# Optimization experiments

Measured on AMD Instinct MI355X. Metric: run time of the kernel, lower is better.

## Reference

```python
import jax, jax.numpy as jnp
import numpy as np
import math

B, C, H, L, E = 4, 4, 8, 512, 128  # L == win_size + 1


def setup_inputs() -> dict:
    key = jax.random.key(0)
    kq, kk, kv, ks = jax.random.split(key, 4)
    queries = jax.random.normal(kq, (B, C, H, L, E), jnp.float32)
    keys = jax.random.normal(kk, (B, C, H, L, E), jnp.float32)
    values = jax.random.normal(kv, (B, C, H, L, E), jnp.float32)
    sigma = jax.random.normal(ks, (B, C, H, L), jnp.float32)
    # triangular causal mask: True above the diagonal (masked out)
    tri = jnp.triu(jnp.ones((L, L), dtype=bool), k=1)
    attn_mask = jnp.broadcast_to(tri[None, None, None], (B, 1, 1, L, L))
    return {"queries": queries, "keys": keys, "values": values,
            "sigma": sigma, "attn_mask": attn_mask}


def reference(queries, keys, values, sigma, attn_mask):
    Bq, Cq, Hq, Lq, Eq = queries.shape
    scale = 1.0 / math.sqrt(Eq)
    # scores: [B,C,H,L,L]
    scores = jnp.einsum("bchle,bchme->bchlm", queries, keys)
    scores = jnp.where(attn_mask, -jnp.inf, scores)
    attn = scale * scores

    # Gaussian prior from learned sigma
    sig = jax.nn.sigmoid(sigma * 5.0) + 1e-5
    sig = jnp.power(3.0, sig) - 1.0            # [B,C,H,L]
    sig = sig[..., None]                        # [B,C,H,L,1]
    idx = jnp.arange(Lq, dtype=queries.dtype)
    dist = jnp.abs(idx[:, None] - idx[None, :])  # [L,L]
    inv_norm = 1.0 / (math.sqrt(2.0 * math.pi) * sig)
    prior = inv_norm * jnp.exp(-(dist ** 2) / (2.0 * sig ** 2))  # [B,C,H,L,L]

    series = jax.nn.softmax(attn, axis=-1)      # dropout p=0.0 -> identity
    V = jnp.einsum("bchlm,bchme->bchle", series, values)
    sigma_out = jnp.broadcast_to(sig, prior.shape)
    return V, series, prior, sigma_out
```

## Files before the change

### kernel.cpp

```cpp
#include <hip/hip_runtime.h>
#include <math.h>

#define L 512
#define E 128
#define NT 8

typedef __attribute__((ext_vector_type(8))) short bf16x8;
typedef __attribute__((ext_vector_type(4))) float f32x4;
typedef __attribute__((ext_vector_type(4))) unsigned short u16x4;

__device__ __forceinline__ unsigned short bf16_rne(float x) {
  unsigned u = __builtin_bit_cast(unsigned, x);
  unsigned r = u + 0x7FFFu + ((u >> 16) & 1u);
  return (unsigned short)(r >> 16);
}
__device__ __forceinline__ float bf16_to_f(unsigned short h) {
  unsigned u = ((unsigned)h) << 16;
  return __builtin_bit_cast(float, u);
}

__global__ __launch_bounds__(256) void prior_kernel(
    const float* __restrict__ sigma,
    float* __restrict__ prior,
    float* __restrict__ sigma_out) {
  const int half = threadIdx.x >> 7;
  const int t128 = threadIdx.x & 127;
  const int m0 = t128 * 4;
#pragma unroll 4
  for (int i = 0; i < 16; ++i) {
    const int row = blockIdx.x * 32 + i * 2 + half;
    const int l = row & (L - 1);
    const float x = sigma[row];
    const float sg = 1.0f / (1.0f + __expf(-5.0f * x)) + 1e-5f;
    const float sigp = expm1f(sg * 1.0986122886681098f);
    const float inv_norm = 0.3989422804014327f / sigp;
    const float c = -1.0f / (2.0f * sigp * sigp);

    f32x4 pr, so;
    so[0] = so[1] = so[2] = so[3] = sigp;
#pragma unroll
    for (int j = 0; j < 4; ++j) {
      float d = (float)(l - (m0 + j));
      pr[j] = inv_norm * __expf(c * d * d);
    }
    const size_t off = (size_t)row * L + m0;
    __builtin_nontemporal_store(pr, (f32x4*)(prior + off));
    __builtin_nontemporal_store(so, (f32x4*)(sigma_out + off));
  }
}

__global__ __launch_bounds__(256, 2) void attn_kernel(
    const float* __restrict__ Q,
    const float* __restrict__ K,
    const float* __restrict__ V,
    float* __restrict__ outV,
    float* __restrict__ series) {
  const int bch = blockIdx.x;
  const int qt = 7 - blockIdx.y;
  const int tid = threadIdx.x;
  const int w = tid >> 6, lane = tid & 63, r = lane & 15, g = lane >> 4;

  __shared__ char smem[47104];
  char* sK = smem;
  char* sVt = smem + 17408;
  char* sP = smem + 37888;

  const size_t base = (size_t)bch * (L * E);
  const int qbase = qt * 64;
  const float scale = 0.08838834764831845f;

  bf16x8 qh[4], ql[4];
  {
    const float* qrow = Q + base + (size_t)(qbase + 16 * w + r) * E;
#pragma unroll
    for (int ks = 0; ks < 4; ++ks) {
      const int e0 = 32 * ks + 8 * g;
      f32x4 a = *(const f32x4*)(qrow + e0);
      f32x4 b = *(const f32x4*)(qrow + e0 + 4);
#pragma unroll
      for (int j = 0; j < 4; ++j) {
        float xa = a[j] * scale;
        unsigned short ha = bf16_rne(xa);
        qh[ks][j] = (short)ha;
        ql[ks][j] = (short)bf16_rne(xa - bf16_to_f(ha));
        float xb = b[j] * scale;
        unsigned short hb = bf16_rne(xb);
        qh[ks][4 + j] = (short)hb;
        ql[ks][4 + j] = (short)bf16_rne(xb - bf16_to_f(hb));
      }
    }
  }

  f32x4 Sacc[NT][4];
  float srow[4] = {0.f, 0.f, 0.f, 0.f};
  f32x4 Oacc[8];
#pragma unroll
  for (int cb = 0; cb < 8; ++cb) Oacc[cb] = (f32x4){0.f, 0.f, 0.f, 0.f};

#pragma unroll
  for (int t = 0; t < NT; ++t) {
    if (t <= qt) {
      __syncthreads();
#pragma unroll
      for (int i = 0; i < 8; ++i) {
        int f = i * 256 + tid;
        int row = f >> 5;
        int e0 = (f & 31) * 4;
        f32x4 kv = *(const f32x4*)(K + base + (size_t)(t * 64 + row) * E + e0);
        u16x4 h4;
#pragma unroll
        for (int j = 0; j < 4; ++j) h4[j] = bf16_rne(kv[j]);
        *(u16x4*)(sK + row * 272 + e0 * 2) = h4;
      }
#pragma unroll
      for (int bb = 0; bb < 2; ++bb) {
        int bidx = tid + 256 * bb;
        int m0 = (bidx >> 5) * 4;
        int e0 = (bidx & 31) * 4;
        const float* vrow = V + base + (size_t)(t * 64 + m0) * E + e0;
        f32x4 R0 = *(const f32x4*)(vrow);
        f32x4 R1 = *(const f32x4*)(vrow + E);
        f32x4 R2 = *(const f32x4*)(vrow + 2 * E);
        f32x4 R3 = *(const f32x4*)(vrow + 3 * E);
#pragma unroll
        for (int i = 0; i < 4; ++i) {
          u16x4 wv;
          wv[0] = bf16_rne(R0[i]);
          wv[1] = bf16_rne(R1[i]);
          wv[2] = bf16_rne(R2[i]);
          wv[3] = bf16_rne(R3[i]);
          int e = e0 + i;
          int byte = e * 160 + m0 * 2;
          byte ^= ((e >> 2) & 7) << 4;
          *(u16x4*)(sVt + byte) = wv;
        }
      }
      __syncthreads();

#pragma unroll
      for (int cb = 0; cb < 4; ++cb) Sacc[t][cb] = (f32x4){0.f, 0.f, 0.f, 0.f};
#pragma unroll
      for (int ks = 0; ks < 4; ++ks) {
#pragma unroll
        for (int cb = 0; cb < 4; ++cb) {
          const int kb = (16 * cb + r) * 272 + (32 * ks + 8 * g) * 2;
          bf16x8 bh = *(const bf16x8*)(sK + kb);
          f32x4 acc = Sacc[t][cb];
          acc = __builtin_amdgcn_mfma_f32_16x16x32_bf16(qh[ks], bh, acc, 0, 0, 0);
          acc = __builtin_amdgcn_mfma_f32_16x16x32_bf16(ql[ks], bh, acc, 0, 0, 0);
          Sacc[t][cb] = acc;
        }
      }

#pragma unroll
      for (int cb = 0; cb < 4; ++cb)
#pragma unroll
        for (int reg = 0; reg < 4; ++reg) {
          float p = __expf(Sacc[t][cb][reg]);
          if (t == qt && (16 * cb + r) > (16 * w + 4 * g + reg)) p = 0.f;
          Sacc[t][cb][reg] = p;
          srow[reg] += p;
          *(unsigned short*)(sP + (16 * w + 4 * g + reg) * 144 +
                             (16 * cb + r) * 2) = bf16_rne(p);
        }
      asm volatile("s_waitcnt lgkmcnt(0)" ::: "memory");
      __builtin_amdgcn_sched_barrier(0);

#pragma unroll
      for (int ks = 0; ks < 2; ++ks) {
        bf16x8 ap =
            *(const bf16x8*)(sP + (16 * w + r) * 144 + (32 * ks + 8 * g) * 2);
#pragma unroll
        for (int cb = 0; cb < 8; ++cb) {
          int e = 16 * cb + r;
          int byte = e * 160 + (32 * ks + 8 * g) * 2;
          byte ^= ((e >> 2) & 7) << 4;
          bf16x8 bv = *(const bf16x8*)(sVt + byte);
          Oacc[cb] = __builtin_amdgcn_mfma_f32_16x16x32_bf16(ap, bv, Oacc[cb],
                                                             0, 0, 0);
        }
      }
    }
  }

  float inv[4];
#pragma unroll
  for (int off = 1; off <= 8; off <<= 1)
#pragma unroll
    for (int reg = 0; reg < 4; ++reg)
      srow[reg] += __shfl_xor(srow[reg], off, 64);
#pragma unroll
  for (int reg = 0; reg < 4; ++reg) inv[reg] = 1.0f / srow[reg];

#pragma unroll
  for (int t = 0; t < NT; ++t) {
#pragma unroll
    for (int cb = 0; cb < 4; ++cb)
#pragma unroll
      for (int reg = 0; reg < 4; ++reg) {
        size_t off = ((size_t)bch * L + qbase + 16 * w + 4 * g + reg) * L +
                     t * 64 + 16 * cb + r;
        float val = (t <= qt) ? Sacc[t][cb][reg] * inv[reg] : 0.f;
        __builtin_nontemporal_store(val, series + off);
      }
  }

#pragma unroll
  for (int cb = 0; cb < 8; ++cb)
#pragma unroll
    for (int reg = 0; reg < 4; ++reg)
      outV[base + (size_t)(qbase + 16 * w + 4 * g + reg) * E + 16 * cb + r] =
          Oacc[cb][reg] * inv[reg];
}

extern "C" void kernel_launch(void* const* d_in, const int* in_sizes, int n_in,
                              void* d_out, int out_size, void* d_ws,
                              size_t ws_size, hipStream_t stream) {
  const float* Q = (const float*)d_in[0];
  const float* K = (const float*)d_in[1];
  const float* V = (const float*)d_in[2];
  const float* sigma = (const float*)d_in[3];

  float* out = (float*)d_out;
  float* outV = out;
  float* series = out + 8388608;
  float* prior = out + 41943040;
  float* sigma_out = out + 75497472;

  attn_kernel<<<dim3(128, 8), 256, 0, stream>>>(Q, K, V, outV, series);
  prior_kernel<<<dim3(2048), 256, 0, stream>>>(sigma, prior, sigma_out);
}
```

Measured before the change: 526.6 us.

## Fuse prior computation into attention kernel and stage outputs through LDS

```diff
diff --git a/kernel.cpp b/kernel.cpp
--- a/kernel.cpp
+++ b/kernel.cpp
@@ -19,51 +19,24 @@
   return __builtin_bit_cast(float, u);
 }
 
-__global__ __launch_bounds__(256) void prior_kernel(
-    const float* __restrict__ sigma,
-    float* __restrict__ prior,
-    float* __restrict__ sigma_out) {
-  const int half = threadIdx.x >> 7;
-  const int t128 = threadIdx.x & 127;
-  const int m0 = t128 * 4;
-#pragma unroll 4
-  for (int i = 0; i < 16; ++i) {
-    const int row = blockIdx.x * 32 + i * 2 + half;
-    const int l = row & (L - 1);
-    const float x = sigma[row];
-    const float sg = 1.0f / (1.0f + __expf(-5.0f * x)) + 1e-5f;
-    const float sigp = expm1f(sg * 1.0986122886681098f);
-    const float inv_norm = 0.3989422804014327f / sigp;
-    const float c = -1.0f / (2.0f * sigp * sigp);
-
-    f32x4 pr, so;
-    so[0] = so[1] = so[2] = so[3] = sigp;
-#pragma unroll
-    for (int j = 0; j < 4; ++j) {
-      float d = (float)(l - (m0 + j));
-      pr[j] = inv_norm * __expf(c * d * d);
-    }
-    const size_t off = (size_t)row * L + m0;
-    __builtin_nontemporal_store(pr, (f32x4*)(prior + off));
-    __builtin_nontemporal_store(so, (f32x4*)(sigma_out + off));
-  }
-}
-
-__global__ __launch_bounds__(256, 2) void attn_kernel(
+__global__ __launch_bounds__(256, 3) void fused_kernel(
     const float* __restrict__ Q,
     const float* __restrict__ K,
     const float* __restrict__ V,
+    const float* __restrict__ sigma,
     float* __restrict__ outV,
-    float* __restrict__ series) {
+    float* __restrict__ series,
+    float* __restrict__ prior,
+    float* __restrict__ sigma_out) {
   const int bch = blockIdx.x;
   const int qt = 7 - blockIdx.y;
   const int tid = threadIdx.x;
   const int w = tid >> 6, lane = tid & 63, r = lane & 15, g = lane >> 4;
 
-  __shared__ char smem[47104];
+  __shared__ char smem[37888];
   char* sK = smem;
   char* sVt = smem + 17408;
-  char* sP = smem + 37888;
+  char* sP = smem;
 
   const size_t base = (size_t)bch * (L * E);
   const int qbase = qt * 64;
@@ -91,7 +64,7 @@
     }
   }
 
-  f32x4 Sacc[NT][4];
+  unsigned Sp[NT][8];
   float srow[4] = {0.f, 0.f, 0.f, 0.f};
   f32x4 Oacc[8];
 #pragma unroll
@@ -137,32 +110,46 @@
       }
       __syncthreads();
 
-#pragma unroll
-      for (int cb = 0; cb < 4; ++cb) Sacc[t][cb] = (f32x4){0.f, 0.f, 0.f, 0.f};
+      f32x4 Sacc[4];
+#pragma unroll
+      for (int cb = 0; cb < 4; ++cb) Sacc[cb] = (f32x4){0.f, 0.f, 0.f, 0.f};
 #pragma unroll
       for (int ks = 0; ks < 4; ++ks) {
 #pragma unroll
         for (int cb = 0; cb < 4; ++cb) {
           const int kb = (16 * cb + r) * 272 + (32 * ks + 8 * g) * 2;
           bf16x8 bh = *(const bf16x8*)(sK + kb);
-          f32x4 acc = Sacc[t][cb];
+          f32x4 acc = Sacc[cb];
           acc = __builtin_amdgcn_mfma_f32_16x16x32_bf16(qh[ks], bh, acc, 0, 0, 0);
           acc = __builtin_amdgcn_mfma_f32_16x16x32_bf16(ql[ks], bh, acc, 0, 0, 0);
-          Sacc[t][cb] = acc;
-        }
-      }
-
+          Sacc[cb] = acc;
+        }
+      }
+
+      unsigned short h[4][4];
 #pragma unroll
       for (int cb = 0; cb < 4; ++cb)
 #pragma unroll
         for (int reg = 0; reg < 4; ++reg) {
-          float p = __expf(Sacc[t][cb][reg]);
+          float p = __expf(Sacc[cb][reg]);
           if (t == qt && (16 * cb + r) > (16 * w + 4 * g + reg)) p = 0.f;
-          Sacc[t][cb][reg] = p;
           srow[reg] += p;
+          h[cb][reg] = bf16_rne(p);
+        }
+#pragma unroll
+      for (int cb = 0; cb < 4; ++cb) {
+        Sp[t][2 * cb + 0] = (unsigned)h[cb][0] | ((unsigned)h[cb][1] << 16);
+        Sp[t][2 * cb + 1] = (unsigned)h[cb][2] | ((unsigned)h[cb][3] << 16);
+      }
+
+      __syncthreads();
+
+#pragma unroll
+      for (int cb = 0; cb < 4; ++cb)
+#pragma unroll
+        for (int reg = 0; reg < 4; ++reg)
           *(unsigned short*)(sP + (16 * w + 4 * g + reg) * 144 +
-                             (16 * cb + r) * 2) = bf16_rne(p);
-        }
+                             (16 * cb + r) * 2) = h[cb][reg];
       asm volatile("s_waitcnt lgkmcnt(0)" ::: "memory");
       __builtin_amdgcn_sched_barrier(0);
 
@@ -192,25 +179,107 @@
 #pragma unroll
   for (int reg = 0; reg < 4; ++reg) inv[reg] = 1.0f / srow[reg];
 
+  __syncthreads();
+
+  float* sInvW = (float*)(smem + 36864) + 16 * w;
+  if (r == 0) {
+#pragma unroll
+    for (int reg = 0; reg < 4; ++reg) sInvW[4 * g + reg] = inv[reg];
+  }
+
 #pragma unroll
   for (int t = 0; t < NT; ++t) {
-#pragma unroll
-    for (int cb = 0; cb < 4; ++cb)
-#pragma unroll
-      for (int reg = 0; reg < 4; ++reg) {
-        size_t off = ((size_t)bch * L + qbase + 16 * w + 4 * g + reg) * L +
-                     t * 64 + 16 * cb + r;
-        float val = (t <= qt) ? Sacc[t][cb][reg] * inv[reg] : 0.f;
-        __builtin_nontemporal_store(val, series + off);
-      }
-  }
-
+    if (t <= qt) {
+#pragma unroll
+      for (int cb = 0; cb < 4; ++cb)
+#pragma unroll
+        for (int j = 0; j < 2; ++j) {
+          unsigned pk = Sp[t][2 * cb + j];
+          *(unsigned short*)(sP + (16 * w + 4 * g + 2 * j) * 144 +
+                             (16 * cb + r) * 2) = (unsigned short)(pk & 0xFFFF);
+          *(unsigned short*)(sP + (16 * w + 4 * g + 2 * j + 1) * 144 +
+                             (16 * cb + r) * 2) = (unsigned short)(pk >> 16);
+        }
+      asm volatile("s_waitcnt lgkmcnt(0)" ::: "memory");
+      __builtin_amdgcn_sched_barrier(0);
+#pragma unroll
+      for (int a = 0; a < 2; ++a) {
+        int rw = 8 * a + (lane >> 3);
+        float iv = sInvW[rw];
+#pragma unroll
+        for (int b = 0; b < 2; ++b) {
+          int m0 = 32 * b + (lane & 7) * 4;
+          u16x4 pv = *(const u16x4*)(sP + (16 * w + rw) * 144 + m0 * 2);
+          f32x4 o;
+          o[0] = bf16_to_f(pv[0]) * iv;
+          o[1] = bf16_to_f(pv[1]) * iv;
+          o[2] = bf16_to_f(pv[2]) * iv;
+          o[3] = bf16_to_f(pv[3]) * iv;
+          __builtin_nontemporal_store(
+              o, (f32x4*)(series + ((size_t)bch * L + qbase + 16 * w + rw) * L +
+                          t * 64 + m0));
+        }
+      }
+    } else {
+      f32x4 z = (f32x4){0.f, 0.f, 0.f, 0.f};
+#pragma unroll
+      for (int a = 0; a < 2; ++a) {
+        int rw = 8 * a + (lane >> 3);
+#pragma unroll
+        for (int b = 0; b < 2; ++b) {
+          int m0 = 32 * b + (lane & 7) * 4;
+          __builtin_nontemporal_store(
+              z, (f32x4*)(series + ((size_t)bch * L + qbase + 16 * w + rw) * L +
+                          t * 64 + m0));
+        }
+      }
+    }
+  }
+
+  __syncthreads();
+
+  float* sOw = (float*)(smem + w * 9472);
 #pragma unroll
   for (int cb = 0; cb < 8; ++cb)
 #pragma unroll
     for (int reg = 0; reg < 4; ++reg)
-      outV[base + (size_t)(qbase + 16 * w + 4 * g + reg) * E + 16 * cb + r] =
-          Oacc[cb][reg] * inv[reg];
+      sOw[(4 * g + reg) * 132 + 16 * cb + r] = Oacc[cb][reg] * inv[reg];
+  asm volatile("s_waitcnt lgkmcnt(0)" ::: "memory");
+  __builtin_amdgcn_sched_barrier(0);
+#pragma unroll
+  for (int a = 0; a < 2; ++a) {
+    int rw = 8 * a + (lane >> 3);
+#pragma unroll
+    for (int j = 0; j < 4; ++j) {
+      int e0 = 32 * j + (lane & 7) * 4;
+      f32x4 o = *(const f32x4*)(sOw + rw * 132 + e0);
+      __builtin_nontemporal_store(
+          o, (f32x4*)(outV + base + (size_t)(qbase + 16 * w + rw) * E + e0));
+    }
+  }
+
+#pragma unroll 4
+  for (int i = 0; i < 32; ++i) {
+    int f = i * 256 + tid;
+    int rowl = f >> 7;
+    int m0 = (f & 127) * 4;
+    int l = qbase + rowl;
+    float x = sigma[bch * L + l];
+    float sg = 1.0f / (1.0f + __expf(-5.0f * x)) + 1e-5f;
+    float sigp = expm1f(sg * 1.0986122886681098f);
+    float inv_norm = 0.3989422804014327f / sigp;
+    float c = -1.0f / (2.0f * sigp * sigp);
+    f32x4 pr, so;
+    so[0] = so[1] = so[2] = so[3] = sigp;
+#pragma unroll
+    for (int j = 0; j < 4; ++j) {
+      float d = (float)(l - (m0 + j));
+      pr[j] = inv_norm * __expf(c * d * d);
+    }
+    size_t off = ((size_t)bch * L + l) * L + m0;
+    __builtin_nontemporal_store(pr, (f32x4*)(prior + off));
+    __builtin_nontemporal_store(so, (f32x4*)(sigma_out + off));
+  }
 }
 
 extern "C" void kernel_launch(void* const* d_in, const int* in_sizes, int n_in,
@@ -227,6 +296,6 @@
   float* prior = out + 41943040;
   float* sigma_out = out + 75497472;
 
-  attn_kernel<<<dim3(128, 8), 256, 0, stream>>>(Q, K, V, outV, series);
-  prior_kernel<<<dim3(2048), 256, 0, stream>>>(sigma, prior, sigma_out);
+  fused_kernel<<<dim3(128, 8), 256, 0, stream>>>(Q, K, V, sigma, outV, series,
+                                                 prior, sigma_out);
 }
```

New measurement: 540.9 us. +2.7%, slower.
